# Optimization experiments

Hardware: AMD Instinct MI355X
Metric: run time of the kernel (lower is better)

## Reference

```python
import jax, jax.numpy as jnp
import numpy as np

B, N, HS, NH = 32, 256, 768, 32
D = HS // NH  # 24


def setup_inputs() -> dict:
    key = jax.random.key(0)
    ks = jax.random.split(key, 20)
    s = 0.02
    inp = {
        "hidden_states": jax.random.normal(ks[0], (B, N, HS), jnp.float32),
        "attention_bias": jax.random.normal(ks[1], (B, NH, N, N), jnp.float32),
        "delta_pos": jax.random.normal(ks[2], (B, N, N, 3), jnp.float32),
        "attention_mask": jnp.ones((B, N), jnp.float32),
        "Wi": jax.random.normal(ks[3], (HS, HS), jnp.float32) * s,
        "bi": jnp.zeros((HS,), jnp.float32),
        "Wq": jax.random.normal(ks[4], (HS, HS), jnp.float32) * s,
        "bq": jnp.zeros((HS,), jnp.float32),
        "Wk": jax.random.normal(ks[5], (HS, HS), jnp.float32) * s,
        "bk": jnp.zeros((HS,), jnp.float32),
        "Wv": jax.random.normal(ks[6], (HS, HS), jnp.float32) * s,
        "bv": jnp.zeros((HS,), jnp.float32),
        "Wf1": jax.random.normal(ks[7], (1, HS), jnp.float32) * s,
        "bf1": jnp.zeros((1,), jnp.float32),
        "Wf2": jax.random.normal(ks[8], (1, HS), jnp.float32) * s,
        "bf2": jnp.zeros((1,), jnp.float32),
        "Wf3": jax.random.normal(ks[9], (1, HS), jnp.float32) * s,
        "bf3": jnp.zeros((1,), jnp.float32),
    }
    return inp


def reference(hidden_states, attention_bias, delta_pos, attention_mask,
              Wi, bi, Wq, bq, Wk, bk, Wv, bv, Wf1, bf1, Wf2, bf2, Wf3, bf3):
    b, n, hs = hidden_states.shape
    nh = NH
    d = hs // nh
    denoise_scaling = d ** (-0.5)
    scale = np.sqrt(denoise_scaling).astype(np.float32)

    # mask: (B,N) -> additive (B,1,1,N)
    neg = ((1.0 - attention_mask) * -100000.0)[:, None, None, :]

    h = jax.nn.gelu(hidden_states @ Wi.T + bi, approximate=False)
    q = (h @ Wq.T + bq).reshape(b, n, nh, d).transpose(0, 2, 1, 3) * scale
    k = (h @ Wk.T + bk).reshape(b, n, nh, d).transpose(0, 2, 1, 3) * scale
    v = (h @ Wv.T + bv).reshape(b, n, nh, d).transpose(0, 2, 1, 3)

    scores = jnp.einsum('bhid,bhjd->bhij', q, k) + attention_bias + neg
    probs = jax.nn.softmax(scores, axis=-1)  # dropout = identity at eval

    # x[b,i,c,h,d] = sum_j probs[b,h,i,j] * delta_pos[b,i,j,c] * v[b,h,j,d]
    x = jnp.einsum('bhij,bijc,bhjd->bichd', probs, delta_pos, v)
    x = x.reshape(b, n, 3, hs)

    f1 = x[:, :, 0, :] @ Wf1.T + bf1  # (B,N,1)
    f2 = x[:, :, 1, :] @ Wf2.T + bf2
    f3 = x[:, :, 2, :] @ Wf3.T + bf3
    return jnp.concatenate([f1, f2, f3], axis=-1).astype(jnp.float32)
```

## Files before the change

kernel.cpp:

```cpp
#include <hip/hip_runtime.h>
#include <hip/hip_fp16.h>

#define B_  32
#define N_  256
#define HS_ 768
#define NH_ 32
#define D_  24
#define M_  (B_*N_)
#define QKVN 2304

typedef unsigned short us8 __attribute__((ext_vector_type(8)));
typedef unsigned short us4v __attribute__((ext_vector_type(4)));
typedef _Float16 f16x8 __attribute__((ext_vector_type(8)));
typedef float f32x4 __attribute__((ext_vector_type(4)));

__device__ __forceinline__ unsigned short f2h(float x){
  return __half_as_ushort(__float2half(x));
}
__device__ __forceinline__ float h2f(unsigned short u){
  return __half2float(__ushort_as_half(u));
}
__device__ __forceinline__ void gload16(const void* g, void* l){
  __builtin_amdgcn_global_load_lds(
      (const __attribute__((address_space(1))) void*)g,
      (__attribute__((address_space(3))) void*)l, 16, 0, 0);
}
__device__ __forceinline__ void pin4(float4 &v){
  asm volatile("" : "+v"(v.x), "+v"(v.y), "+v"(v.z), "+v"(v.w));
}

__global__ __launch_bounds__(256) void cvt_kernel(const float* __restrict__ in,
                                                  unsigned short* __restrict__ out, int n4){
  int i = blockIdx.x*256 + threadIdx.x;
  if (i >= n4) return;
  float4 v = ((const float4*)in)[i];
  ushort4 o;
  o.x = f2h(v.x); o.y = f2h(v.y); o.z = f2h(v.z); o.w = f2h(v.w);
  ((ushort4*)out)[i] = o;
}

__global__ __launch_bounds__(256) void gemm128_kernel(
    const unsigned short* __restrict__ A, const unsigned short* __restrict__ W,
    const float* __restrict__ b0, const float* __restrict__ b1, const float* __restrict__ b2,
    unsigned short* __restrict__ C, int M, int N, int K, int dogelu)
{
  __shared__ unsigned short As[128*64];
  __shared__ unsigned short Bs[128*64];
  int gswz = blockIdx.x;
  int chunkg = gridDim.x >> 3;
  int bid = (gswz & 7)*chunkg + (gswz >> 3);
  int tid = threadIdx.x;
  int nT = N >> 7;
  int tm = bid / nT;
  int tn = bid - tm*nT;
  int which = (tn << 7) / 768;
  const float* bp = (which == 0) ? b0 : (which == 1) ? b1 : b2;
  bp -= which * 768;
  int wave = tid >> 6, lane = tid & 63;
  int wm = (wave >> 1) << 6;
  int wn = (wave & 1) << 6;
  int fr = lane & 15;
  int g  = lane >> 4;

  size_t aoff[4], woff[4];
  int ldsb[4];
#pragma unroll
  for (int s4 = 0; s4 < 4; s4++){
    int ob = s4*4096 + tid*16;
    int r  = ob >> 7;
    int p  = (ob >> 4) & 7;
    int l  = p ^ (r & 7);
    aoff[s4] = ((size_t)(tm*128 + r)*K)*2 + l*16;
    woff[s4] = ((size_t)(tn*128 + r)*K)*2 + l*16;
    ldsb[s4] = s4*4096 + wave*1024;
  }
  const char* Ab = (const char*)A;
  const char* Wb = (const char*)W;
  char* AsB = (char*)As;
  char* BsB = (char*)Bs;

  f32x4 acc[4][4];
#pragma unroll
  for (int m = 0; m < 4; m++)
#pragma unroll
    for (int n = 0; n < 4; n++) acc[m][n] = (f32x4){0.f,0.f,0.f,0.f};

  for (int k0 = 0; k0 < K; k0 += 64){
    size_t kb = (size_t)k0*2;
#pragma unroll
    for (int s4 = 0; s4 < 4; s4++) gload16(Ab + aoff[s4] + kb, AsB + ldsb[s4]);
#pragma unroll
    for (int s4 = 0; s4 < 4; s4++) gload16(Wb + woff[s4] + kb, BsB + ldsb[s4]);
    __syncthreads();

    f16x8 af[4], bf[4];
#pragma unroll
    for (int m = 0; m < 4; m++){
      int row = wm + m*16 + fr;
      af[m] = __builtin_bit_cast(f16x8, *(const us8*)(AsB + row*128 + ((g ^ (row & 7))*16)));
    }
#pragma unroll
    for (int n = 0; n < 4; n++){
      int row = wn + n*16 + fr;
      bf[n] = __builtin_bit_cast(f16x8, *(const us8*)(BsB + row*128 + ((g ^ (row & 7))*16)));
    }
#pragma unroll
    for (int m = 0; m < 4; m++)
#pragma unroll
      for (int n = 0; n < 4; n++)
        acc[m][n] = __builtin_amdgcn_mfma_f32_16x16x32_f16(af[m], bf[n], acc[m][n], 0, 0, 0);

#pragma unroll
    for (int m = 0; m < 4; m++){
      int row = wm + m*16 + fr;
      af[m] = __builtin_bit_cast(f16x8, *(const us8*)(AsB + row*128 + (((g+4) ^ (row & 7))*16)));
    }
#pragma unroll
    for (int n = 0; n < 4; n++){
      int row = wn + n*16 + fr;
      bf[n] = __builtin_bit_cast(f16x8, *(const us8*)(BsB + row*128 + (((g+4) ^ (row & 7))*16)));
    }
#pragma unroll
    for (int m = 0; m < 4; m++)
#pragma unroll
      for (int n = 0; n < 4; n++)
        acc[m][n] = __builtin_amdgcn_mfma_f32_16x16x32_f16(af[m], bf[n], acc[m][n], 0, 0, 0);
    __syncthreads();
  }

#pragma unroll
  for (int n = 0; n < 4; n++){
    int col = tn*128 + wn + n*16 + fr;
    float bv = bp[col];
#pragma unroll
    for (int m = 0; m < 4; m++){
      int row = tm*128 + wm + m*16 + g*4;
#pragma unroll
      for (int q = 0; q < 4; q++){
        float v = acc[m][n][q] + bv;
        if (dogelu) v = 0.5f*v*(1.0f + erff(v*0.70710678118654752f));
        C[(size_t)(row + q)*N + col] = f2h(v);
      }
    }
  }
}

__global__ __launch_bounds__(256) void prep_kernel(
    const unsigned short* __restrict__ qkv, const float* __restrict__ mask,
    const float* __restrict__ Wf1, const float* __restrict__ Wf2, const float* __restrict__ Wf3,
    unsigned short* __restrict__ u16,
    float* __restrict__ negv)
{
  int bh = blockIdx.x;
  int h = bh & 31, b = bh >> 5;
  int j = threadIdx.x;
  const unsigned short* vr = qkv + (size_t)(b*N_ + j)*QKVN + 1536 + h*D_;
  us8 v0 = *(const us8*)(vr);
  us8 v1 = *(const us8*)(vr + 8);
  us8 v2 = *(const us8*)(vr + 16);
  const float* w1 = Wf1 + h*D_;
  const float* w2 = Wf2 + h*D_;
  const float* w3 = Wf3 + h*D_;
  float u0 = 0.f, u1 = 0.f, u2 = 0.f;
#pragma unroll
  for (int e = 0; e < 8; e++){
    float va = h2f(v0[e]), vb2 = h2f(v1[e]), vc = h2f(v2[e]);
    u0 += va*w1[e] + vb2*w1[8+e] + vc*w1[16+e];
    u1 += va*w2[e] + vb2*w2[8+e] + vc*w2[16+e];
    u2 += va*w3[e] + vb2*w3[8+e] + vc*w3[16+e];
  }
  us4v o = {f2h(u0), f2h(u1), f2h(u2), 0};
  *(us4v*)(u16 + ((size_t)bh*N_ + j)*4) = o;
  if (h == 0) negv[b*N_ + j] = (1.0f - mask[b*N_ + j]) * -100000.0f;
}

#define SCALE 0.20412414523193154f
#define INVSCALE 4.898979485566356f
#define M0 16.0f
__global__ __launch_bounds__(256, 4) void attn_kernel(
    const unsigned short* __restrict__ qkv,
    const float* __restrict__ bias,
    const unsigned short* __restrict__ u16,
    const float* __restrict__ negv,
    const float* __restrict__ dp,
    float* __restrict__ fpart)
{
  int gswz = blockIdx.x;
  int lin = (gswz & 7)*128 + (gswz >> 3);
  int b = lin >> 5, ic = (lin >> 1) & 15, jh = lin & 1;
  int i0 = ic*16, j00 = jh*128;
  int t = threadIdx.x;
  int wave = t >> 6, lane = t & 63;
  int ch = wave, fr = lane & 15, g = lane >> 4;

  __shared__ __align__(16) char smem[35840];
  char* zp = smem + 32768;
  char* scratch = smem + 33792;

  int bsrc[2];
#pragma unroll
  for (int k = 0; k < 2; k++){
    int a = k*4096 + t*16;
    int row = a >> 9;
    int pc = (a >> 4) & 31;
    int lc = pc ^ (row & 7);
    bsrc[k] = row*1024 + lc*16;
  }
  const char* bb0 = (const char*)bias
      + ((size_t)(b*NH_)*65536 + (size_t)i0*256 + j00)*4;

  const char* sbase[2]; int sstep[2];
#pragma unroll
  for (int k = 0; k < 2; k++){
    int G = k*256 + t;
    if (G < 384){
      int c = G >> 7, r = G & 127;
      sbase[k] = (const char*)qkv + ((size_t)(b*N_ + j00 + r)*4608 + 1536 + c*16);
      sstep[k] = 48;
    } else if (G < 432){
      int x = G - 384; int i = x/3; int c = x - i*3;
      sbase[k] = (const char*)qkv + ((size_t)(b*N_ + i0 + i)*4608 + c*16);
      sstep[k] = 48;
    } else {
      int kk = (G < 496) ? (G - 432) : 63;
      sbase[k] = (const char*)u16 + ((size_t)(b*NH_)*2048 + jh*1024 + kk*16);
      sstep[k] = 2048;
    }
  }

  #define ISSUE(hh) do { \
    int _par = (hh) & 1; \
    const char* _bp = bb0 + (size_t)(hh)*262144; \
    gload16(_bp + bsrc[0], smem + _par*8192 + wave*1024); \
    gload16(_bp + bsrc[1], smem + _par*8192 + 4096 + wave*1024); \
    gload16(sbase[0] + (size_t)(hh)*sstep[0], smem + 16384 + _par*8192 + wave*1024); \
    gload16(sbase[1] + (size_t)(hh)*sstep[1], smem + 16384 + _par*8192 + 4096 + wave*1024); \
  } while(0)

  float4 nv[2]; float4 dpre[6];
  {
    const float* nb = negv + b*N_ + j00;
#pragma unroll
    for (int jt = 0; jt < 2; jt++)
      nv[jt] = *(const float4*)(nb + ch*32 + jt*16 + g*4);
    const float* dpb = dp + (size_t)(b*N_ + i0 + fr)*768;
#pragma unroll
    for (int jt = 0; jt < 2; jt++){
      const float4* dq = (const float4*)(dpb + (size_t)(j00 + ch*32 + jt*16 + g*4)*3);
      dpre[jt*3+0] = dq[0]; dpre[jt*3+1] = dq[1]; dpre[jt*3+2] = dq[2];
    }
  }
  asm volatile("s_waitcnt vmcnt(0)" ::: "memory");
  pin4(nv[0]); pin4(nv[1]);
#pragma unroll
  for (int k = 0; k < 6; k++) pin4(dpre[k]);

  ISSUE(0);
  gload16(negv + b*N_, scratch);
  if (t < 128) *(us8*)(zp + t*16) = (us8){0,0,0,0,0,0,0,0};
  asm volatile("s_waitcnt lgkmcnt(0)" ::: "memory");

  int swz = (fr & 7) << 4;
  float4* fp4 = (float4*)fpart;
  size_t fbase = (((size_t)(b*16 + ic)*2 + jh)*32)*64 + ch*16 + fr;

#pragma unroll 1
  for (int h = 0; h < 32; h++){
    asm volatile("s_waitcnt vmcnt(1)" ::: "memory");
    __builtin_amdgcn_s_barrier();
    if (h < 31) ISSUE(h+1);

    const char* bslot = smem + (h & 1)*8192;
    const char* sslot = smem + 16384 + (h & 1)*8192;

    const char* qa = (g < 3) ? (sslot + 6144 + fr*48 + g*16) : (zp + fr*16);
    f16x8 qf = __builtin_bit_cast(f16x8, *(const us8*)qa);

    float S = 0.f, a0 = 0.f, a1 = 0.f, a2 = 0.f;
#pragma unroll
    for (int jt = 0; jt < 2; jt++){
      int j0l = ch*32 + jt*16 + g*4;
      float4 bv = *(const float4*)(bslot + fr*512 + ((j0l*4) ^ swz));
      f32x4 cin;
      cin[0] = (bv.x + nv[jt].x)*INVSCALE;
      cin[1] = (bv.y + nv[jt].y)*INVSCALE;
      cin[2] = (bv.z + nv[jt].z)*INVSCALE;
      cin[3] = (bv.w + nv[jt].w)*INVSCALE;
      int krow = ch*32 + jt*16 + fr;
      const char* ka = (g < 3) ? (sslot + g*2048 + krow*16) : (zp + krow*16);
      f16x8 kf = __builtin_bit_cast(f16x8, *(const us8*)ka);
      f32x4 sv = __builtin_amdgcn_mfma_f32_16x16x32_f16(kf, qf, cin, 0, 0, 0);
      float p0 = __expf(fmaf(sv[0], SCALE, -M0));
      float p1 = __expf(fmaf(sv[1], SCALE, -M0));
      float p2 = __expf(fmaf(sv[2], SCALE, -M0));
      float p3 = __expf(fmaf(sv[3], SCALE, -M0));
      S += p0 + p1 + p2 + p3;
      us8 ua = *(const us8*)(sslot + 6912 + j0l*8);
      us8 ub = *(const us8*)(sslot + 6912 + j0l*8 + 16);
      float4 d0 = dpre[jt*3], d1 = dpre[jt*3+1], d2 = dpre[jt*3+2];
      a0 += p0*h2f(ua[0])*d0.x + p1*h2f(ua[4])*d0.w + p2*h2f(ub[0])*d1.z + p3*h2f(ub[4])*d2.y;
      a1 += p0*h2f(ua[1])*d0.y + p1*h2f(ua[5])*d1.x + p2*h2f(ub[1])*d1.w + p3*h2f(ub[5])*d2.z;
      a2 += p0*h2f(ua[2])*d0.z + p1*h2f(ua[6])*d1.y + p2*h2f(ub[2])*d2.x + p3*h2f(ub[6])*d2.w;
    }
    S  += __shfl_xor(S, 16);  S  += __shfl_xor(S, 32);
    a0 += __shfl_xor(a0, 16); a0 += __shfl_xor(a0, 32);
    a1 += __shfl_xor(a1, 16); a1 += __shfl_xor(a1, 32);
    a2 += __shfl_xor(a2, 16); a2 += __shfl_xor(a2, 32);
    if (lane < 16)
      fp4[fbase + (size_t)h*64] = make_float4(S, a0, a1, a2);
  }
  asm volatile("s_waitcnt vmcnt(0)" ::: "memory");
  #undef ISSUE
}

__global__ __launch_bounds__(256) void final_kernel(const float* __restrict__ fpart,
    const float* __restrict__ bf1, const float* __restrict__ bf2, const float* __restrict__ bf3,
    float* __restrict__ out)
{
  int idx = blockIdx.x*256 + threadIdx.x;
  int b = idx >> 8, i = idx & 255;
  int ic = i >> 4, ii = i & 15;
  const float4* fp4 = (const float4*)fpart;
  size_t base = ((size_t)(b*16 + ic)*2)*2048 + ii;
  float acc0 = 0.f, acc1 = 0.f, acc2 = 0.f;
#pragma unroll 4
  for (int h = 0; h < 32; h++){
    float S = 0.f, A0 = 0.f, A1 = 0.f, A2 = 0.f;
#pragma unroll
    for (int jh = 0; jh < 2; jh++){
#pragma unroll
      for (int ch = 0; ch < 4; ch++){
        float4 v = fp4[base + (size_t)jh*2048 + (size_t)h*64 + ch*16];
        S += v.x; A0 += v.y; A1 += v.z; A2 += v.w;
      }
    }
    float rs = 1.0f / S;
    acc0 += A0*rs; acc1 += A1*rs; acc2 += A2*rs;
  }
  float* op = out + (size_t)idx*3;
  op[0] = acc0 + bf1[0];
  op[1] = acc1 + bf2[0];
  op[2] = acc2 + bf3[0];
}

extern "C" void kernel_launch(void* const* d_in, const int* in_sizes, int n_in,
                              void* d_out, int out_size, void* d_ws, size_t ws_size,
                              hipStream_t stream)
{
  const float* X    = (const float*)d_in[0];
  const float* bias = (const float*)d_in[1];
  const float* dp   = (const float*)d_in[2];
  const float* mask = (const float*)d_in[3];
  const float* Wi   = (const float*)d_in[4];
  const float* bi   = (const float*)d_in[5];
  const float* Wq   = (const float*)d_in[6];
  const float* bq   = (const float*)d_in[7];
  const float* Wk   = (const float*)d_in[8];
  const float* bk   = (const float*)d_in[9];
  const float* Wv   = (const float*)d_in[10];
  const float* bv   = (const float*)d_in[11];
  const float* Wf1  = (const float*)d_in[12];
  const float* bf1  = (const float*)d_in[13];
  const float* Wf2  = (const float*)d_in[14];
  const float* bf2  = (const float*)d_in[15];
  const float* Wf3  = (const float*)d_in[16];
  const float* bf3  = (const float*)d_in[17];
  float* out = (float*)d_out;

  unsigned short* xb   = (unsigned short*)d_ws;
  unsigned short* wib  = xb   + (size_t)M_*HS_;
  unsigned short* wqb  = wib  + (size_t)HS_*HS_;
  unsigned short* wkb  = wqb  + (size_t)HS_*HS_;
  unsigned short* wvb  = wkb  + (size_t)HS_*HS_;
  unsigned short* hb   = wvb  + (size_t)HS_*HS_;
  unsigned short* qkvb = hb   + (size_t)M_*HS_;
  unsigned short* u16a = qkvb + (size_t)M_*QKVN;
  float* negv  = (float*)(u16a + (size_t)B_*NH_*N_*4);
  float* fpart = negv + (size_t)B_*N_;

  {
    int n4 = M_*HS_/4;
    cvt_kernel<<<n4/256, 256, 0, stream>>>(X, xb, n4);
    int w4 = HS_*HS_/4;
    cvt_kernel<<<w4/256, 256, 0, stream>>>(Wi, wib, w4);
    cvt_kernel<<<w4/256, 256, 0, stream>>>(Wq, wqb, w4);
    cvt_kernel<<<w4/256, 256, 0, stream>>>(Wk, wkb, w4);
    cvt_kernel<<<w4/256, 256, 0, stream>>>(Wv, wvb, w4);
  }

  gemm128_kernel<<<(M_/128)*(HS_/128), 256, 0, stream>>>(xb, wib, bi, bi, bi, hb, M_, HS_, HS_, 1);
  gemm128_kernel<<<(M_/128)*(QKVN/128), 256, 0, stream>>>(hb, wqb, bq, bk, bv, qkvb, M_, QKVN, HS_, 0);

  prep_kernel<<<B_*NH_, 256, 0, stream>>>(qkvb, mask, Wf1, Wf2, Wf3, u16a, negv);

  attn_kernel<<<B_*16*2, 256, 0, stream>>>(qkvb, bias, u16a, negv, dp, fpart);

  final_kernel<<<(B_*N_)/256, 256, 0, stream>>>(fpart, bf1, bf2, bf3, out);
}
```

Measured before the change: 212.2 us.

## Store QKV in head-major layout for contiguous per-head attention loads

```diff
diff --git a/kernel.cpp b/kernel.cpp
--- a/kernel.cpp
+++ b/kernel.cpp
@@ -42,7 +42,7 @@
 __global__ __launch_bounds__(256) void gemm128_kernel(
     const unsigned short* __restrict__ A, const unsigned short* __restrict__ W,
     const float* __restrict__ b0, const float* __restrict__ b1, const float* __restrict__ b2,
-    unsigned short* __restrict__ C, int M, int N, int K, int dogelu)
+    unsigned short* __restrict__ C, int M, int N, int K, int dogelu, int headmajor)
 {
   __shared__ unsigned short As[128*64];
   __shared__ unsigned short Bs[128*64];
@@ -132,21 +132,27 @@
   for (int n = 0; n < 4; n++){
     int col = tn*128 + wn + n*16 + fr;
     float bv = bp[col];
+    int mat = col / 768;
+    int hd  = col - mat*768;
+    int hh  = hd / 24;
+    int dd  = hd - hh*24;
 #pragma unroll
     for (int m = 0; m < 4; m++){
       int row = tm*128 + wm + m*16 + g*4;
+      size_t hmbase = ((size_t)(mat*1024 + (row >> 8)*32 + hh))*6144 + (row & 255)*24 + dd;
 #pragma unroll
       for (int q = 0; q < 4; q++){
         float v = acc[m][n][q] + bv;
         if (dogelu) v = 0.5f*v*(1.0f + erff(v*0.70710678118654752f));
-        C[(size_t)(row + q)*N + col] = f2h(v);
+        if (headmajor) C[hmbase + q*24] = f2h(v);
+        else           C[(size_t)(row + q)*N + col] = f2h(v);
       }
     }
   }
 }
 
 __global__ __launch_bounds__(256) void prep_kernel(
-    const unsigned short* __restrict__ qkv, const float* __restrict__ mask,
+    const unsigned short* __restrict__ qkvh, const float* __restrict__ mask,
     const float* __restrict__ Wf1, const float* __restrict__ Wf2, const float* __restrict__ Wf3,
     unsigned short* __restrict__ u16,
     float* __restrict__ negv)
@@ -154,7 +160,7 @@
   int bh = blockIdx.x;
   int h = bh & 31, b = bh >> 5;
   int j = threadIdx.x;
-  const unsigned short* vr = qkv + (size_t)(b*N_ + j)*QKVN + 1536 + h*D_;
+  const unsigned short* vr = qkvh + ((size_t)(2*1024 + b*32 + h))*6144 + j*24;
   us8 v0 = *(const us8*)(vr);
   us8 v1 = *(const us8*)(vr + 8);
   us8 v2 = *(const us8*)(vr + 16);
@@ -178,7 +184,7 @@
 #define INVSCALE 4.898979485566356f
 #define M0 16.0f
 __global__ __launch_bounds__(256, 4) void attn_kernel(
-    const unsigned short* __restrict__ qkv,
+    const unsigned short* __restrict__ qkvh,
     const float* __restrict__ bias,
     const unsigned short* __restrict__ u16,
     const float* __restrict__ negv,
@@ -209,23 +215,18 @@
   const char* bb0 = (const char*)bias
       + ((size_t)(b*NH_)*65536 + (size_t)i0*256 + j00)*4;
 
+  const char* qkvhB = (const char*)qkvh;
+  const char* kbase0 = qkvhB + ((size_t)(1024 + b*32))*12288 + jh*6144;
+  const char* qbase0 = qkvhB + ((size_t)(b*32))*12288 + (size_t)i0*48;
+  const char* ubase0 = (const char*)u16 + ((size_t)(b*NH_))*2048 + jh*1024;
   const char* sbase[2]; int sstep[2];
 #pragma unroll
   for (int k = 0; k < 2; k++){
     int G = k*256 + t;
-    if (G < 384){
-      int c = G >> 7, r = G & 127;
-      sbase[k] = (const char*)qkv + ((size_t)(b*N_ + j00 + r)*4608 + 1536 + c*16);
-      sstep[k] = 48;
-    } else if (G < 432){
-      int x = G - 384; int i = x/3; int c = x - i*3;
-      sbase[k] = (const char*)qkv + ((size_t)(b*N_ + i0 + i)*4608 + c*16);
-      sstep[k] = 48;
-    } else {
-      int kk = (G < 496) ? (G - 432) : 63;
-      sbase[k] = (const char*)u16 + ((size_t)(b*NH_)*2048 + jh*1024 + kk*16);
-      sstep[k] = 2048;
-    }
+    if (G < 384){ sbase[k] = kbase0 + G*16;        sstep[k] = 12288; }
+    else if (G < 432){ sbase[k] = qbase0 + (G-384)*16; sstep[k] = 12288; }
+    else if (G < 496){ sbase[k] = ubase0 + (G-432)*16; sstep[k] = 2048; }
+    else { sbase[k] = ubase0; sstep[k] = 2048; }
   }
 
   #define ISSUE(hh) do { \
@@ -287,7 +288,7 @@
       cin[2] = (bv.z + nv[jt].z)*INVSCALE;
       cin[3] = (bv.w + nv[jt].w)*INVSCALE;
       int krow = ch*32 + jt*16 + fr;
-      const char* ka = (g < 3) ? (sslot + g*2048 + krow*16) : (zp + krow*16);
+      const char* ka = sslot + krow*48 + g*16;
       f16x8 kf = __builtin_bit_cast(f16x8, *(const us8*)ka);
       f32x4 sv = __builtin_amdgcn_mfma_f32_16x16x32_f16(kf, qf, cin, 0, 0, 0);
       float p0 = __expf(fmaf(sv[0], SCALE, -M0));
@@ -373,8 +374,8 @@
   unsigned short* wkb  = wqb  + (size_t)HS_*HS_;
   unsigned short* wvb  = wkb  + (size_t)HS_*HS_;
   unsigned short* hb   = wvb  + (size_t)HS_*HS_;
-  unsigned short* qkvb = hb   + (size_t)M_*HS_;
-  unsigned short* u16a = qkvb + (size_t)M_*QKVN;
+  unsigned short* qkvh = hb   + (size_t)M_*HS_;
+  unsigned short* u16a = qkvh + (size_t)3*1024*6144;
   float* negv  = (float*)(u16a + (size_t)B_*NH_*N_*4);
   float* fpart = negv + (size_t)B_*N_;
 
@@ -388,12 +389,12 @@
     cvt_kernel<<<w4/256, 256, 0, stream>>>(Wv, wvb, w4);
   }
 
-  gemm128_kernel<<<(M_/128)*(HS_/128), 256, 0, stream>>>(xb, wib, bi, bi, bi, hb, M_, HS_, HS_, 1);
-  gemm128_kernel<<<(M_/128)*(QKVN/128), 256, 0, stream>>>(hb, wqb, bq, bk, bv, qkvb, M_, QKVN, HS_, 0);
-
-  prep_kernel<<<B_*NH_, 256, 0, stream>>>(qkvb, mask, Wf1, Wf2, Wf3, u16a, negv);
-
-  attn_kernel<<<B_*16*2, 256, 0, stream>>>(qkvb, bias, u16a, negv, dp, fpart);
+  gemm128_kernel<<<(M_/128)*(HS_/128), 256, 0, stream>>>(xb, wib, bi, bi, bi, hb, M_, HS_, HS_, 1, 0);
+  gemm128_kernel<<<(M_/128)*(QKVN/128), 256, 0, stream>>>(hb, wqb, bq, bk, bv, qkvh, M_, QKVN, HS_, 0, 1);
+
+  prep_kernel<<<B_*NH_, 256, 0, stream>>>(qkvh, mask, Wf1, Wf2, Wf3, u16a, negv);
+
+  attn_kernel<<<B_*16*2, 256, 0, stream>>>(qkvh, bias, u16a, negv, dp, fpart);
 
   final_kernel<<<(B_*N_)/256, 256, 0, stream>>>(fpart, bf1, bf2, bf3, out);
 }
```

Result: faster. 183.7 us (-13.4%).
